# Optimization experiments

Measured on AMD Instinct MI355X. Metric: run time of the kernel, lower is better.

The kernel has to match this reference:

```python
import jax, jax.numpy as jnp
import numpy as np

EPS_F = 1e-6   # epsilon_F global in original repo
GAMMA = 0.8
K = 5
BN_EPS = 1e-5
M = 128
N = 100000
E = 1600000
MY = 10

def setup_inputs() -> dict:
    key = jax.random.key(0)
    ks = jax.random.split(key, 6)
    X = jax.random.normal(ks[0], (M, N), dtype=jnp.float32)
    # xavier_uniform for F: limit = sqrt(6/(m+m))
    lim = float(np.sqrt(6.0 / (M + M)))
    F_mat = jax.random.uniform(ks[1], (M, M), dtype=jnp.float32, minval=-lim, maxval=lim)
    B = (1.0 / np.sqrt(M)) * jax.random.normal(ks[2], (MY, M), dtype=jnp.float32)
    bn_weight = jnp.ones((M,), dtype=jnp.float32)
    bn_bias = jnp.zeros((M,), dtype=jnp.float32)
    edge_val = jax.random.uniform(ks[3], (E,), dtype=jnp.float32)
    edge_row = jax.random.randint(ks[4], (E,), 0, N, dtype=jnp.int64 if jax.config.jax_enable_x64 else jnp.int32)
    edge_col = jax.random.randint(ks[5], (E,), 0, N, dtype=jnp.int64 if jax.config.jax_enable_x64 else jnp.int32)
    return {"X": X, "F_mat": F_mat, "B": B, "bn_weight": bn_weight,
            "bn_bias": bn_bias, "edge_val": edge_val,
            "edge_row": edge_row, "edge_col": edge_col}

def reference(X, F_mat, B, bn_weight, bn_bias, edge_val, edge_row, edge_col):
    n = X.shape[1]
    # normalized Gram matrix g(F) = F^T F / (||F^T F||_fro + eps)
    FF = F_mat.T @ F_mat                       # [m, m]
    G = FF / (jnp.linalg.norm(FF) + EPS_F)
    X_first = X                                # [m, n]

    def step(Xc, _):
        Y = Xc.T                               # [n, m]
        # SpMM: (S_t @ Y)[r] += val * Y[c]
        SY = jax.ops.segment_sum(edge_val[:, None] * Y[edge_col], edge_row,
                                 num_segments=n)   # [n, m]
        Xn = GAMMA * (G @ SY.T) + X_first          # [m, n]
        return Xn, None

    Xk, _ = jax.lax.scan(step, X, None, length=K)
    out = Xk.T                                 # [n, m]
    # BatchNorm1d over feature dim (training-mode batch stats); dropout omitted (eval)
    mu = out.mean(axis=0)
    var = out.var(axis=0)
    out = (out - mu) * jax.lax.rsqrt(var + BN_EPS) * bn_weight + bn_bias
    return out @ B.T                           # [n, m_y]
```

## Files before the change

### kernel.cpp

```cpp
#include <hip/hip_runtime.h>
#include <math.h>

#define MDIM 128
#define MY 10
#define GAMMA 0.8f
#define KITER 5

__device__ __forceinline__ float bf2f(unsigned short h) {
    return __uint_as_float(((unsigned int)h) << 16);
}
__device__ __forceinline__ unsigned short f2bf(float f) {
    unsigned int u = __float_as_uint(f);
    u += 0x7fffu + ((u >> 16) & 1u);
    return (unsigned short)(u >> 16);
}

__global__ void k_transpose(const float* __restrict__ X, float* __restrict__ Y0,
                            unsigned short* __restrict__ Y0h, int n) {
    __shared__ float tile[32][33];
    int r0 = blockIdx.x * 32;
    int f0 = blockIdx.y * 32;
    int tx = threadIdx.x, ty = threadIdx.y;
    #pragma unroll
    for (int i = 0; i < 32; i += 8) {
        tile[ty + i][tx] = X[(size_t)(f0 + ty + i) * n + (r0 + tx)];
    }
    __syncthreads();
    #pragma unroll
    for (int i = 0; i < 32; i += 8) {
        float v = tile[tx][ty + i];
        Y0[(size_t)(r0 + ty + i) * MDIM + (f0 + tx)] = v;
        Y0h[(size_t)(r0 + ty + i) * MDIM + (f0 + tx)] = f2bf(v);
    }
}

__global__ void k_gram(const float* __restrict__ F, float* __restrict__ FF,
                       float* __restrict__ normAcc) {
    int i = blockIdx.x, j = threadIdx.x;
    float acc = 0.f;
    for (int k = 0; k < MDIM; ++k)
        acc = fmaf(F[k * MDIM + i], F[k * MDIM + j], acc);
    FF[i * MDIM + j] = acc;
    __shared__ float red[MDIM];
    red[j] = acc * acc;
    __syncthreads();
    for (int s = 64; s > 0; s >>= 1) {
        if (j < s) red[j] += red[j + s];
        __syncthreads();
    }
    if (j == 0) atomicAdd(normAcc, red[0]);
}

__global__ void k_gnorm(const float* __restrict__ FF, const float* __restrict__ normAcc,
                        float* __restrict__ G) {
    int idx = blockIdx.x * 256 + threadIdx.x;
    float s = GAMMA / (sqrtf(*normAcc) + 1e-6f);
    G[idx] = FF[idx] * s;
}

__global__ void k_hist(const int* __restrict__ erow, int* __restrict__ cnt, int E) {
    int e = blockIdx.x * 256 + threadIdx.x;
    if (e < E) atomicAdd(&cnt[erow[e]], 1);
}

__global__ void k_scan1(const int* __restrict__ cnt, int* __restrict__ blockSums, int n) {
    int tid = threadIdx.x;
    int base = blockIdx.x * 1024 + tid * 4;
    int s = 0;
    if (base + 3 < n) {
        int4 v = *(const int4*)&cnt[base];
        s = v.x + v.y + v.z + v.w;
    } else {
        for (int i = 0; i < 4; ++i)
            if (base + i < n) s += cnt[base + i];
    }
    __shared__ int red[256];
    red[tid] = s;
    __syncthreads();
    for (int st = 128; st > 0; st >>= 1) {
        if (tid < st) red[tid] += red[tid + st];
        __syncthreads();
    }
    if (tid == 0) blockSums[blockIdx.x] = red[0];
}

__global__ void k_scan2(int* __restrict__ blockSums, int* __restrict__ row_off,
                        int nb, int n) {
    __shared__ int s[256];
    int tid = threadIdx.x;
    int v = (tid < nb) ? blockSums[tid] : 0;
    s[tid] = v;
    __syncthreads();
    for (int off = 1; off < 256; off <<= 1) {
        int t = (tid >= off) ? s[tid - off] : 0;
        __syncthreads();
        s[tid] += t;
        __syncthreads();
    }
    if (tid < nb) blockSums[tid] = s[tid] - v;
    if (tid == 0) row_off[n] = s[255];
}

__global__ void k_scan3(const int* __restrict__ cnt, const int* __restrict__ blockOff,
                        int* __restrict__ row_off, int n) {
    int tid = threadIdx.x;
    int base = blockIdx.x * 1024 + tid * 4;
    int v[4];
    #pragma unroll
    for (int i = 0; i < 4; ++i) v[i] = (base + i < n) ? cnt[base + i] : 0;
    int local = v[0] + v[1] + v[2] + v[3];
    __shared__ int s[256];
    s[tid] = local;
    __syncthreads();
    for (int off = 1; off < 256; off <<= 1) {
        int t = (tid >= off) ? s[tid - off] : 0;
        __syncthreads();
        s[tid] += t;
        __syncthreads();
    }
    int excl = s[tid] - local + blockOff[blockIdx.x];
    #pragma unroll
    for (int i = 0; i < 4; ++i) {
        if (base + i < n) { row_off[base + i] = excl; excl += v[i]; }
    }
}

__global__ void k_scatter(const int* __restrict__ erow, const int* __restrict__ ecol,
                          const float* __restrict__ eval_, int* __restrict__ cursor,
                          int2* __restrict__ csr_cv, int E) {
    int e = blockIdx.x * 256 + threadIdx.x;
    if (e < E) {
        int r = erow[e];
        int pos = atomicAdd(&cursor[r], 1);
        csr_cv[pos] = make_int2(ecol[e], __float_as_int(eval_[e]));
    }
}

__global__ void __launch_bounds__(256, 8) k_fused(const unsigned short* __restrict__ Yh,
                                                  const int* __restrict__ row_off,
                                                  const int2* __restrict__ csr_cv,
                                                  const float* __restrict__ G,
                                                  const float* __restrict__ Y0,
                                                  float* __restrict__ Yout,
                                                  unsigned short* __restrict__ Yhout,
                                                  float* __restrict__ stats,
                                                  int writeH, int writeF, int n) {
    __shared__ float sSY[32 * MDIM];
    int tid = threadIdx.x;
    int ty = tid >> 5;
    int tx = tid & 31;
    int rbase = blockIdx.x * 32;

    for (int i = 0; i < 4; ++i) {
        int rloc = ty * 4 + i;
        int e0 = row_off[rbase + rloc];
        int e1 = row_off[rbase + rloc + 1];
        float4 a = make_float4(0.f, 0.f, 0.f, 0.f);
        int e = e0;
        for (; e + 4 <= e1; e += 4) {
            int2 p0 = csr_cv[e + 0];
            int2 p1 = csr_cv[e + 1];
            int2 p2 = csr_cv[e + 2];
            int2 p3 = csr_cv[e + 3];
            ushort4 h0 = *(const ushort4*)&Yh[(size_t)p0.x * MDIM + tx * 4];
            ushort4 h1 = *(const ushort4*)&Yh[(size_t)p1.x * MDIM + tx * 4];
            ushort4 h2 = *(const ushort4*)&Yh[(size_t)p2.x * MDIM + tx * 4];
            ushort4 h3 = *(const ushort4*)&Yh[(size_t)p3.x * MDIM + tx * 4];
            float v0 = __int_as_float(p0.y);
            float v1 = __int_as_float(p1.y);
            float v2 = __int_as_float(p2.y);
            float v3 = __int_as_float(p3.y);
            a.x = fmaf(v0, bf2f(h0.x), a.x);
            a.y = fmaf(v0, bf2f(h0.y), a.y);
            a.z = fmaf(v0, bf2f(h0.z), a.z);
            a.w = fmaf(v0, bf2f(h0.w), a.w);
            a.x = fmaf(v1, bf2f(h1.x), a.x);
            a.y = fmaf(v1, bf2f(h1.y), a.y);
            a.z = fmaf(v1, bf2f(h1.z), a.z);
            a.w = fmaf(v1, bf2f(h1.w), a.w);
            a.x = fmaf(v2, bf2f(h2.x), a.x);
            a.y = fmaf(v2, bf2f(h2.y), a.y);
            a.z = fmaf(v2, bf2f(h2.z), a.z);
            a.w = fmaf(v2, bf2f(h2.w), a.w);
            a.x = fmaf(v3, bf2f(h3.x), a.x);
            a.y = fmaf(v3, bf2f(h3.y), a.y);
            a.z = fmaf(v3, bf2f(h3.z), a.z);
            a.w = fmaf(v3, bf2f(h3.w), a.w);
        }
        for (; e < e1; ++e) {
            int2 p = csr_cv[e];
            float v = __int_as_float(p.y);
            ushort4 h = *(const ushort4*)&Yh[(size_t)p.x * MDIM + tx * 4];
            a.x = fmaf(v, bf2f(h.x), a.x);
            a.y = fmaf(v, bf2f(h.y), a.y);
            a.z = fmaf(v, bf2f(h.z), a.z);
            a.w = fmaf(v, bf2f(h.w), a.w);
        }
        *(float4*)&sSY[rloc * MDIM + tx * 4] = a;
    }

    size_t r0 = (size_t)rbase + ty * 4;
    int f0 = tx * 4;
    float4 acc[4];
    #pragma unroll
    for (int i = 0; i < 4; ++i) acc[i] = make_float4(0.f, 0.f, 0.f, 0.f);

    for (int j = 0; j < MDIM; j += 4) {
        float4 g0 = *(const float4*)&G[(j + 0) * MDIM + f0];
        float4 g1 = *(const float4*)&G[(j + 1) * MDIM + f0];
        float4 g2 = *(const float4*)&G[(j + 2) * MDIM + f0];
        float4 g3 = *(const float4*)&G[(j + 3) * MDIM + f0];
        #pragma unroll
        for (int i = 0; i < 4; ++i) {
            float4 sr = *(const float4*)&sSY[(ty * 4 + i) * MDIM + j];
            acc[i].x = fmaf(sr.x, g0.x, acc[i].x);
            acc[i].y = fmaf(sr.x, g0.y, acc[i].y);
            acc[i].z = fmaf(sr.x, g0.z, acc[i].z);
            acc[i].w = fmaf(sr.x, g0.w, acc[i].w);
            acc[i].x = fmaf(sr.y, g1.x, acc[i].x);
            acc[i].y = fmaf(sr.y, g1.y, acc[i].y);
            acc[i].z = fmaf(sr.y, g1.z, acc[i].z);
            acc[i].w = fmaf(sr.y, g1.w, acc[i].w);
            acc[i].x = fmaf(sr.z, g2.x, acc[i].x);
            acc[i].y = fmaf(sr.z, g2.y, acc[i].y);
            acc[i].z = fmaf(sr.z, g2.z, acc[i].z);
            acc[i].w = fmaf(sr.z, g2.w, acc[i].w);
            acc[i].x = fmaf(sr.w, g3.x, acc[i].x);
            acc[i].y = fmaf(sr.w, g3.y, acc[i].y);
            acc[i].z = fmaf(sr.w, g3.z, acc[i].z);
            acc[i].w = fmaf(sr.w, g3.w, acc[i].w);
        }
    }

    float4 bs = make_float4(0.f, 0.f, 0.f, 0.f);
    float4 bq = make_float4(0.f, 0.f, 0.f, 0.f);
    #pragma unroll
    for (int i = 0; i < 4; ++i) {
        float4 y0 = *(const float4*)&Y0[(r0 + i) * MDIM + f0];
        float4 o;
        o.x = acc[i].x + y0.x;
        o.y = acc[i].y + y0.y;
        o.z = acc[i].z + y0.z;
        o.w = acc[i].w + y0.w;
        if (writeF) {
            *(float4*)&Yout[(r0 + i) * MDIM + f0] = o;
            bs.x += o.x; bs.y += o.y; bs.z += o.z; bs.w += o.w;
            bq.x = fmaf(o.x, o.x, bq.x);
            bq.y = fmaf(o.y, o.y, bq.y);
            bq.z = fmaf(o.z, o.z, bq.z);
            bq.w = fmaf(o.w, o.w, bq.w);
        }
        if (writeH) {
            ushort4 h;
            h.x = f2bf(o.x);
            h.y = f2bf(o.y);
            h.z = f2bf(o.z);
            h.w = f2bf(o.w);
            *(ushort4*)&Yhout[(r0 + i) * MDIM + f0] = h;
        }
    }

    if (writeF) {
        __syncthreads();
        *(float4*)&sSY[ty * MDIM + f0] = bs;
        *(float4*)&sSY[8 * MDIM + ty * MDIM + f0] = bq;
        __syncthreads();
        if (tid < MDIM) {
            float a = 0.f, b = 0.f;
            #pragma unroll
            for (int t = 0; t < 8; ++t) {
                a += sSY[t * MDIM + tid];
                b += sSY[8 * MDIM + t * MDIM + tid];
            }
            atomicAdd(&stats[tid], a);
            atomicAdd(&stats[MDIM + tid], b);
        }
    }
}

__global__ void k_finalize(const float* __restrict__ stats, const float* __restrict__ B,
                           const float* __restrict__ bnw, const float* __restrict__ bnb,
                           float* __restrict__ Bs, float* __restrict__ cvec, int n) {
    int f = threadIdx.x;
    float inv_n = 1.f / (float)n;
    float mu = stats[f] * inv_n;
    float var = stats[MDIM + f] * inv_n - mu * mu;
    float rs = rsqrtf(var + 1e-5f);
    float sw = rs * bnw[f];
    float cv = bnb[f] - mu * sw;
    __shared__ float red[MDIM];
    for (int o = 0; o < MY; ++o) {
        float b = B[o * MDIM + f];
        Bs[o * MDIM + f] = b * sw;
        red[f] = b * cv;
        __syncthreads();
        for (int s = 64; s > 0; s >>= 1) {
            if (f < s) red[f] += red[f + s];
            __syncthreads();
        }
        if (f == 0) cvec[o] = red[0];
        __syncthreads();
    }
}

__global__ void __launch_bounds__(256) k_project(const float* __restrict__ Y,
                                                 const float* __restrict__ Bs,
                                                 const float* __restrict__ cvec,
                                                 float* __restrict__ out, int n) {
    __shared__ float yt[16 * 129];
    __shared__ float sB[MY * 129];
    __shared__ float sc[MY];
    int tid = threadIdx.x;
    size_t rbase = (size_t)blockIdx.x * 16;
    for (int idx = tid; idx < 16 * MDIM; idx += 256) {
        int r = idx >> 7, f = idx & 127;
        yt[r * 129 + f] = Y[(rbase + r) * MDIM + f];
    }
    for (int idx = tid; idx < MY * MDIM; idx += 256) {
        int o = idx >> 7, f = idx & 127;
        sB[o * 129 + f] = Bs[idx];
    }
    if (tid < MY) sc[tid] = cvec[tid];
    __syncthreads();
    if (tid < 16 * MY) {
        int r = tid / MY, o = tid % MY;
        float acc = sc[o];
        for (int f = 0; f < MDIM; ++f)
            acc = fmaf(yt[r * 129 + f], sB[o * 129 + f], acc);
        out[(rbase + r) * MY + o] = acc;
    }
}

extern "C" void kernel_launch(void* const* d_in, const int* in_sizes, int n_in,
                              void* d_out, int out_size, void* d_ws, size_t ws_size,
                              hipStream_t stream) {
    const float* X    = (const float*)d_in[0];
    const float* F    = (const float*)d_in[1];
    const float* B    = (const float*)d_in[2];
    const float* bnw  = (const float*)d_in[3];
    const float* bnb  = (const float*)d_in[4];
    const float* ev   = (const float*)d_in[5];
    const int*   erow = (const int*)d_in[6];
    const int*   ecol = (const int*)d_in[7];
    float* out = (float*)d_out;
    const int n = in_sizes[0] / MDIM;
    const int E = in_sizes[5];

    char* w = (char*)d_ws;
    size_t off = 0;
    auto carve = [&](size_t bytes) -> void* {
        void* p = w + off;
        off += (bytes + 255) & ~(size_t)255;
        return p;
    };
    float*          Y0    = (float*)carve((size_t)n * MDIM * 4);
    float*          Ycur  = (float*)carve((size_t)n * MDIM * 4);
    unsigned short* Yh_a  = (unsigned short*)carve((size_t)n * MDIM * 2);
    unsigned short* Yh_b  = (unsigned short*)carve((size_t)n * MDIM * 2);
    float* FF        = (float*)carve(MDIM * MDIM * 4);
    float* G         = (float*)carve(MDIM * MDIM * 4);
    int2*  csr_cv    = (int2*)carve((size_t)E * 8);
    int*   row_off   = (int*)carve((size_t)(n + 1) * 4);
    int*   cursor    = (int*)carve((size_t)n * 4);
    int*   cnt       = (int*)carve((size_t)n * 4);
    int*   blockSums = (int*)carve(1024 * 4);
    float* normAcc   = (float*)carve(4);
    float* stats     = (float*)carve(2 * MDIM * 4);
    float* Bs        = (float*)carve(MY * MDIM * 4);
    float* cvec      = (float*)carve(MY * 4);
    (void)ws_size;

    hipMemsetAsync(cnt, 0, (size_t)n * 4, stream);
    hipMemsetAsync(normAcc, 0, 4, stream);
    hipMemsetAsync(stats, 0, 2 * MDIM * 4, stream);

    k_transpose<<<dim3(n / 32, MDIM / 32), dim3(32, 8), 0, stream>>>(X, Y0, Yh_a, n);
    k_gram<<<MDIM, MDIM, 0, stream>>>(F, FF, normAcc);
    k_gnorm<<<MDIM * MDIM / 256, 256, 0, stream>>>(FF, normAcc, G);

    const int nb = (n + 1023) / 1024;
    k_hist<<<(E + 255) / 256, 256, 0, stream>>>(erow, cnt, E);
    k_scan1<<<nb, 256, 0, stream>>>(cnt, blockSums, n);
    k_scan2<<<1, 256, 0, stream>>>(blockSums, row_off, nb, n);
    k_scan3<<<nb, 256, 0, stream>>>(cnt, blockSums, row_off, n);
    hipMemcpyAsync(cursor, row_off, (size_t)n * 4, hipMemcpyDeviceToDevice, stream);
    k_scatter<<<(E + 255) / 256, 256, 0, stream>>>(erow, ecol, ev, cursor, csr_cv, E);

    for (int k = 0; k < KITER; ++k) {
        const unsigned short* hin = (k & 1) ? Yh_b : Yh_a;
        unsigned short*       hout = (k & 1) ? Yh_a : Yh_b;
        int writeH = (k < KITER - 1) ? 1 : 0;
        int writeF = (k == KITER - 1) ? 1 : 0;
        k_fused<<<n / 32, 256, 0, stream>>>(hin, row_off, csr_cv, G, Y0, Ycur, hout,
                                            stats, writeH, writeF, n);
    }

    k_finalize<<<1, MDIM, 0, stream>>>(stats, B, bnw, bnb, Bs, cvec, n);
    k_project<<<n / 16, 256, 0, stream>>>(Ycur, Bs, cvec, out, n);
}
```

Measured before the change: 920.4 us.

## Bucket CSR edges within each row by column chunk and prescale column byte offsets

```diff
diff --git a/kernel.cpp b/kernel.cpp
--- a/kernel.cpp
+++ b/kernel.cpp
@@ -5,6 +5,9 @@
 #define MY 10
 #define GAMMA 0.8f
 #define KITER 5
+#define CSHIFT 13
+#define CCHUNK 13
+#define SCAN_BLK 8192
 
 __device__ __forceinline__ float bf2f(unsigned short h) {
     return __uint_as_float(((unsigned int)h) << 16);
@@ -58,21 +61,25 @@
     G[idx] = FF[idx] * s;
 }
 
-__global__ void k_hist(const int* __restrict__ erow, int* __restrict__ cnt, int E) {
+__global__ void k_hist(const int* __restrict__ erow, const int* __restrict__ ecol,
+                       int* __restrict__ cnt, int E) {
     int e = blockIdx.x * 256 + threadIdx.x;
-    if (e < E) atomicAdd(&cnt[erow[e]], 1);
-}
-
-__global__ void k_scan1(const int* __restrict__ cnt, int* __restrict__ blockSums, int n) {
+    if (e < E) atomicAdd(&cnt[erow[e] * CCHUNK + (ecol[e] >> CSHIFT)], 1);
+}
+
+__global__ void k_scan1(const int* __restrict__ cnt, int* __restrict__ blockSums, int nC) {
     int tid = threadIdx.x;
-    int base = blockIdx.x * 1024 + tid * 4;
+    int base = blockIdx.x * SCAN_BLK + tid * 32;
     int s = 0;
-    if (base + 3 < n) {
-        int4 v = *(const int4*)&cnt[base];
-        s = v.x + v.y + v.z + v.w;
+    if (base + 31 < nC) {
+        #pragma unroll
+        for (int i = 0; i < 8; ++i) {
+            int4 v = *(const int4*)&cnt[base + i * 4];
+            s += v.x + v.y + v.z + v.w;
+        }
     } else {
-        for (int i = 0; i < 4; ++i)
-            if (base + i < n) s += cnt[base + i];
+        for (int i = 0; i < 32; ++i)
+            if (base + i < nC) s += cnt[base + i];
     }
     __shared__ int red[256];
     red[tid] = s;
@@ -84,8 +91,8 @@
     if (tid == 0) blockSums[blockIdx.x] = red[0];
 }
 
-__global__ void k_scan2(int* __restrict__ blockSums, int* __restrict__ row_off,
-                        int nb, int n) {
+__global__ void k_scan2(int* __restrict__ blockSums, int* __restrict__ rc_off,
+                        int nb, int nC) {
     __shared__ int s[256];
     int tid = threadIdx.x;
     int v = (tid < nb) ? blockSums[tid] : 0;
@@ -98,17 +105,19 @@
         __syncthreads();
     }
     if (tid < nb) blockSums[tid] = s[tid] - v;
-    if (tid == 0) row_off[n] = s[255];
+    if (tid == 0) rc_off[nC] = s[255];
 }
 
 __global__ void k_scan3(const int* __restrict__ cnt, const int* __restrict__ blockOff,
-                        int* __restrict__ row_off, int n) {
+                        int* __restrict__ rc_off, int nC) {
     int tid = threadIdx.x;
-    int base = blockIdx.x * 1024 + tid * 4;
-    int v[4];
-    #pragma unroll
-    for (int i = 0; i < 4; ++i) v[i] = (base + i < n) ? cnt[base + i] : 0;
-    int local = v[0] + v[1] + v[2] + v[3];
+    int base = blockIdx.x * SCAN_BLK + tid * 32;
+    int v[32];
+    #pragma unroll
+    for (int i = 0; i < 32; ++i) v[i] = (base + i < nC) ? cnt[base + i] : 0;
+    int local = 0;
+    #pragma unroll
+    for (int i = 0; i < 32; ++i) local += v[i];
     __shared__ int s[256];
     s[tid] = local;
     __syncthreads();
@@ -120,8 +129,8 @@
     }
     int excl = s[tid] - local + blockOff[blockIdx.x];
     #pragma unroll
-    for (int i = 0; i < 4; ++i) {
-        if (base + i < n) { row_off[base + i] = excl; excl += v[i]; }
+    for (int i = 0; i < 32; ++i) {
+        if (base + i < nC) { rc_off[base + i] = excl; excl += v[i]; }
     }
 }
 
@@ -131,13 +140,14 @@
     int e = blockIdx.x * 256 + threadIdx.x;
     if (e < E) {
         int r = erow[e];
-        int pos = atomicAdd(&cursor[r], 1);
-        csr_cv[pos] = make_int2(ecol[e], __float_as_int(eval_[e]));
+        int c = ecol[e];
+        int pos = atomicAdd(&cursor[r * CCHUNK + (c >> CSHIFT)], 1);
+        csr_cv[pos] = make_int2(c << 8, __float_as_int(eval_[e]));
     }
 }
 
 __global__ void __launch_bounds__(256, 8) k_fused(const unsigned short* __restrict__ Yh,
-                                                  const int* __restrict__ row_off,
+                                                  const int* __restrict__ rc_off,
                                                   const int2* __restrict__ csr_cv,
                                                   const float* __restrict__ G,
                                                   const float* __restrict__ Y0,
@@ -150,11 +160,13 @@
     int ty = tid >> 5;
     int tx = tid & 31;
     int rbase = blockIdx.x * 32;
+    const char* yb = (const char*)Yh;
+    int lbo = tx * 8;
 
     for (int i = 0; i < 4; ++i) {
         int rloc = ty * 4 + i;
-        int e0 = row_off[rbase + rloc];
-        int e1 = row_off[rbase + rloc + 1];
+        int e0 = rc_off[(rbase + rloc) * CCHUNK];
+        int e1 = rc_off[(rbase + rloc) * CCHUNK + CCHUNK];
         float4 a = make_float4(0.f, 0.f, 0.f, 0.f);
         int e = e0;
         for (; e + 4 <= e1; e += 4) {
@@ -162,10 +174,10 @@
             int2 p1 = csr_cv[e + 1];
             int2 p2 = csr_cv[e + 2];
             int2 p3 = csr_cv[e + 3];
-            ushort4 h0 = *(const ushort4*)&Yh[(size_t)p0.x * MDIM + tx * 4];
-            ushort4 h1 = *(const ushort4*)&Yh[(size_t)p1.x * MDIM + tx * 4];
-            ushort4 h2 = *(const ushort4*)&Yh[(size_t)p2.x * MDIM + tx * 4];
-            ushort4 h3 = *(const ushort4*)&Yh[(size_t)p3.x * MDIM + tx * 4];
+            ushort4 h0 = *(const ushort4*)(yb + (size_t)(p0.x + lbo));
+            ushort4 h1 = *(const ushort4*)(yb + (size_t)(p1.x + lbo));
+            ushort4 h2 = *(const ushort4*)(yb + (size_t)(p2.x + lbo));
+            ushort4 h3 = *(const ushort4*)(yb + (size_t)(p3.x + lbo));
             float v0 = __int_as_float(p0.y);
             float v1 = __int_as_float(p1.y);
             float v2 = __int_as_float(p2.y);
@@ -190,7 +202,7 @@
         for (; e < e1; ++e) {
             int2 p = csr_cv[e];
             float v = __int_as_float(p.y);
-            ushort4 h = *(const ushort4*)&Yh[(size_t)p.x * MDIM + tx * 4];
+            ushort4 h = *(const ushort4*)(yb + (size_t)(p.x + lbo));
             a.x = fmaf(v, bf2f(h.x), a.x);
             a.y = fmaf(v, bf2f(h.y), a.y);
             a.z = fmaf(v, bf2f(h.z), a.z);
@@ -345,6 +357,7 @@
     float* out = (float*)d_out;
     const int n = in_sizes[0] / MDIM;
     const int E = in_sizes[5];
+    const int nC = n * CCHUNK;
 
     char* w = (char*)d_ws;
     size_t off = 0;
@@ -360,9 +373,9 @@
     float* FF        = (float*)carve(MDIM * MDIM * 4);
     float* G         = (float*)carve(MDIM * MDIM * 4);
     int2*  csr_cv    = (int2*)carve((size_t)E * 8);
-    int*   row_off   = (int*)carve((size_t)(n + 1) * 4);
-    int*   cursor    = (int*)carve((size_t)n * 4);
-    int*   cnt       = (int*)carve((size_t)n * 4);
+    int*   rc_off    = (int*)carve((size_t)(nC + 1) * 4);
+    int*   cursor    = (int*)carve((size_t)nC * 4);
+    int*   cnt       = (int*)carve((size_t)nC * 4);
     int*   blockSums = (int*)carve(1024 * 4);
     float* normAcc   = (float*)carve(4);
     float* stats     = (float*)carve(2 * MDIM * 4);
@@ -370,7 +383,7 @@
     float* cvec      = (float*)carve(MY * 4);
     (void)ws_size;
 
-    hipMemsetAsync(cnt, 0, (size_t)n * 4, stream);
+    hipMemsetAsync(cnt, 0, (size_t)nC * 4, stream);
     hipMemsetAsync(normAcc, 0, 4, stream);
     hipMemsetAsync(stats, 0, 2 * MDIM * 4, stream);
 
@@ -378,12 +391,12 @@
     k_gram<<<MDIM, MDIM, 0, stream>>>(F, FF, normAcc);
     k_gnorm<<<MDIM * MDIM / 256, 256, 0, stream>>>(FF, normAcc, G);
 
-    const int nb = (n + 1023) / 1024;
-    k_hist<<<(E + 255) / 256, 256, 0, stream>>>(erow, cnt, E);
-    k_scan1<<<nb, 256, 0, stream>>>(cnt, blockSums, n);
-    k_scan2<<<1, 256, 0, stream>>>(blockSums, row_off, nb, n);
-    k_scan3<<<nb, 256, 0, stream>>>(cnt, blockSums, row_off, n);
-    hipMemcpyAsync(cursor, row_off, (size_t)n * 4, hipMemcpyDeviceToDevice, stream);
+    const int nb = (nC + SCAN_BLK - 1) / SCAN_BLK;
+    k_hist<<<(E + 255) / 256, 256, 0, stream>>>(erow, ecol, cnt, E);
+    k_scan1<<<nb, 256, 0, stream>>>(cnt, blockSums, nC);
+    k_scan2<<<1, 256, 0, stream>>>(blockSums, rc_off, nb, nC);
+    k_scan3<<<nb, 256, 0, stream>>>(cnt, blockSums, rc_off, nC);
+    hipMemcpyAsync(cursor, rc_off, (size_t)nC * 4, hipMemcpyDeviceToDevice, stream);
     k_scatter<<<(E + 255) / 256, 256, 0, stream>>>(erow, ecol, ev, cursor, csr_cv, E);
 
     for (int k = 0; k < KITER; ++k) {
@@ -391,7 +404,7 @@
         unsigned short*       hout = (k & 1) ? Yh_a : Yh_b;
         int writeH = (k < KITER - 1) ? 1 : 0;
         int writeF = (k == KITER - 1) ? 1 : 0;
-        k_fused<<<n / 32, 256, 0, stream>>>(hin, row_off, csr_cv, G, Y0, Ycur, hout,
+        k_fused<<<n / 32, 256, 0, stream>>>(hin, rc_off, csr_cv, G, Y0, Ycur, hout,
                                             stats, writeH, writeF, n);
     }
 
```

After: 934.0 us. About the same (+1.5%).

## Bucket CSR edges by row groups of four and gather with full-wavefront bf16x2 loads

Applied to the files above, without the earlier changes.

```diff
diff --git a/kernel.cpp b/kernel.cpp
--- a/kernel.cpp
+++ b/kernel.cpp
@@ -16,7 +16,8 @@
 }
 
 __global__ void k_transpose(const float* __restrict__ X, float* __restrict__ Y0,
-                            unsigned short* __restrict__ Y0h, int n) {
+                            unsigned short* __restrict__ Y0h,
+                            unsigned short* __restrict__ Yh0, int n) {
     __shared__ float tile[32][33];
     int r0 = blockIdx.x * 32;
     int f0 = blockIdx.y * 32;
@@ -29,8 +30,10 @@
     #pragma unroll
     for (int i = 0; i < 32; i += 8) {
         float v = tile[tx][ty + i];
+        unsigned short h = f2bf(v);
         Y0[(size_t)(r0 + ty + i) * MDIM + (f0 + tx)] = v;
-        Y0h[(size_t)(r0 + ty + i) * MDIM + (f0 + tx)] = f2bf(v);
+        Y0h[(size_t)(r0 + ty + i) * MDIM + (f0 + tx)] = h;
+        Yh0[(size_t)(r0 + ty + i) * MDIM + (f0 + tx)] = h;
     }
 }
 
@@ -125,80 +128,101 @@
     }
 }
 
+__global__ void k_cinit(const int* __restrict__ row_off, int* __restrict__ cursorB, int nbk) {
+    int b = blockIdx.x * 256 + threadIdx.x;
+    if (b < nbk) cursorB[b] = row_off[b << 2];
+}
+
 __global__ void k_scatter(const int* __restrict__ erow, const int* __restrict__ ecol,
-                          const float* __restrict__ eval_, int* __restrict__ cursor,
+                          const float* __restrict__ eval_, int* __restrict__ cursorB,
                           int2* __restrict__ csr_cv, int E) {
     int e = blockIdx.x * 256 + threadIdx.x;
     if (e < E) {
         int r = erow[e];
-        int pos = atomicAdd(&cursor[r], 1);
-        csr_cv[pos] = make_int2(ecol[e], __float_as_int(eval_[e]));
-    }
-}
+        int c = ecol[e];
+        int pos = atomicAdd(&cursorB[r >> 2], 1);
+        csr_cv[pos] = make_int2((c << 8) | (r & 3), __float_as_int(eval_[e]));
+    }
+}
+
+#define EDGE(p, h, A0, A1, A2, A3)                                          \
+    {                                                                       \
+        float v = __int_as_float(p.y);                                      \
+        float f0 = __uint_as_float(((unsigned)h) << 16);                    \
+        float f1 = __uint_as_float(((unsigned)h) & 0xFFFF0000u);            \
+        int rid = __builtin_amdgcn_readfirstlane(p.x) & 3;                  \
+        if (rid == 0)      { A0.x = fmaf(v, f0, A0.x); A0.y = fmaf(v, f1, A0.y); } \
+        else if (rid == 1) { A1.x = fmaf(v, f0, A1.x); A1.y = fmaf(v, f1, A1.y); } \
+        else if (rid == 2) { A2.x = fmaf(v, f0, A2.x); A2.y = fmaf(v, f1, A2.y); } \
+        else               { A3.x = fmaf(v, f0, A3.x); A3.y = fmaf(v, f1, A3.y); } \
+    }
+
+#define GATHER_BUCKET(BK, A0, A1, A2, A3)                                   \
+    {                                                                       \
+        int e  = row_off[(BK) << 2];                                        \
+        int e1 = row_off[((BK) << 2) + 4];                                  \
+        for (; e + 8 <= e1; e += 8) {                                       \
+            int2 p0 = csr_cv[e + 0]; int2 p1 = csr_cv[e + 1];               \
+            int2 p2 = csr_cv[e + 2]; int2 p3 = csr_cv[e + 3];               \
+            int2 p4 = csr_cv[e + 4]; int2 p5 = csr_cv[e + 5];               \
+            int2 p6 = csr_cv[e + 6]; int2 p7 = csr_cv[e + 7];               \
+            unsigned h0 = *(const unsigned*)(yb + (size_t)((p0.x & 0xFFFFFF00) + lbo)); \
+            unsigned h1 = *(const unsigned*)(yb + (size_t)((p1.x & 0xFFFFFF00) + lbo)); \
+            unsigned h2 = *(const unsigned*)(yb + (size_t)((p2.x & 0xFFFFFF00) + lbo)); \
+            unsigned h3 = *(const unsigned*)(yb + (size_t)((p3.x & 0xFFFFFF00) + lbo)); \
+            unsigned h4 = *(const unsigned*)(yb + (size_t)((p4.x & 0xFFFFFF00) + lbo)); \
+            unsigned h5 = *(const unsigned*)(yb + (size_t)((p5.x & 0xFFFFFF00) + lbo)); \
+            unsigned h6 = *(const unsigned*)(yb + (size_t)((p6.x & 0xFFFFFF00) + lbo)); \
+            unsigned h7 = *(const unsigned*)(yb + (size_t)((p7.x & 0xFFFFFF00) + lbo)); \
+            EDGE(p0, h0, A0, A1, A2, A3) EDGE(p1, h1, A0, A1, A2, A3)       \
+            EDGE(p2, h2, A0, A1, A2, A3) EDGE(p3, h3, A0, A1, A2, A3)       \
+            EDGE(p4, h4, A0, A1, A2, A3) EDGE(p5, h5, A0, A1, A2, A3)       \
+            EDGE(p6, h6, A0, A1, A2, A3) EDGE(p7, h7, A0, A1, A2, A3)       \
+        }                                                                   \
+        for (; e < e1; ++e) {                                               \
+            int2 p = csr_cv[e];                                             \
+            unsigned h = *(const unsigned*)(yb + (size_t)((p.x & 0xFFFFFF00) + lbo)); \
+            EDGE(p, h, A0, A1, A2, A3)                                      \
+        }                                                                   \
+    }
 
 __global__ void __launch_bounds__(256, 8) k_fused(const unsigned short* __restrict__ Yh,
                                                   const int* __restrict__ row_off,
                                                   const int2* __restrict__ csr_cv,
                                                   const float* __restrict__ G,
                                                   const float* __restrict__ Y0,
+                                                  const unsigned short* __restrict__ Y0h,
                                                   float* __restrict__ Yout,
                                                   unsigned short* __restrict__ Yhout,
                                                   float* __restrict__ stats,
                                                   int writeH, int writeF, int n) {
     __shared__ float sSY[32 * MDIM];
     int tid = threadIdx.x;
+    int lane = tid & 63;
+    int w = tid >> 6;
+    int rbase = blockIdx.x * 32;
+    const char* yb = (const char*)Yh;
+    int lbo = lane * 4;
+
+    float2 z = make_float2(0.f, 0.f);
+    float2 a0 = z, a1 = z, a2 = z, a3 = z;
+    float2 b0 = z, b1 = z, b2 = z, b3 = z;
+
+    int bk0 = (rbase >> 2) + 2 * w;
+    GATHER_BUCKET(bk0,     a0, a1, a2, a3)
+    GATHER_BUCKET(bk0 + 1, b0, b1, b2, b3)
+
+    *(float2*)&sSY[(w * 8 + 0) * MDIM + lane * 2] = a0;
+    *(float2*)&sSY[(w * 8 + 1) * MDIM + lane * 2] = a1;
+    *(float2*)&sSY[(w * 8 + 2) * MDIM + lane * 2] = a2;
+    *(float2*)&sSY[(w * 8 + 3) * MDIM + lane * 2] = a3;
+    *(float2*)&sSY[(w * 8 + 4) * MDIM + lane * 2] = b0;
+    *(float2*)&sSY[(w * 8 + 5) * MDIM + lane * 2] = b1;
+    *(float2*)&sSY[(w * 8 + 6) * MDIM + lane * 2] = b2;
+    *(float2*)&sSY[(w * 8 + 7) * MDIM + lane * 2] = b3;
+
     int ty = tid >> 5;
     int tx = tid & 31;
-    int rbase = blockIdx.x * 32;
-
-    for (int i = 0; i < 4; ++i) {
-        int rloc = ty * 4 + i;
-        int e0 = row_off[rbase + rloc];
-        int e1 = row_off[rbase + rloc + 1];
-        float4 a = make_float4(0.f, 0.f, 0.f, 0.f);
-        int e = e0;
-        for (; e + 4 <= e1; e += 4) {
-            int2 p0 = csr_cv[e + 0];
-            int2 p1 = csr_cv[e + 1];
-            int2 p2 = csr_cv[e + 2];
-            int2 p3 = csr_cv[e + 3];
-            ushort4 h0 = *(const ushort4*)&Yh[(size_t)p0.x * MDIM + tx * 4];
-            ushort4 h1 = *(const ushort4*)&Yh[(size_t)p1.x * MDIM + tx * 4];
-            ushort4 h2 = *(const ushort4*)&Yh[(size_t)p2.x * MDIM + tx * 4];
-            ushort4 h3 = *(const ushort4*)&Yh[(size_t)p3.x * MDIM + tx * 4];
-            float v0 = __int_as_float(p0.y);
-            float v1 = __int_as_float(p1.y);
-            float v2 = __int_as_float(p2.y);
-            float v3 = __int_as_float(p3.y);
-            a.x = fmaf(v0, bf2f(h0.x), a.x);
-            a.y = fmaf(v0, bf2f(h0.y), a.y);
-            a.z = fmaf(v0, bf2f(h0.z), a.z);
-            a.w = fmaf(v0, bf2f(h0.w), a.w);
-            a.x = fmaf(v1, bf2f(h1.x), a.x);
-            a.y = fmaf(v1, bf2f(h1.y), a.y);
-            a.z = fmaf(v1, bf2f(h1.z), a.z);
-            a.w = fmaf(v1, bf2f(h1.w), a.w);
-            a.x = fmaf(v2, bf2f(h2.x), a.x);
-            a.y = fmaf(v2, bf2f(h2.y), a.y);
-            a.z = fmaf(v2, bf2f(h2.z), a.z);
-            a.w = fmaf(v2, bf2f(h2.w), a.w);
-            a.x = fmaf(v3, bf2f(h3.x), a.x);
-            a.y = fmaf(v3, bf2f(h3.y), a.y);
-            a.z = fmaf(v3, bf2f(h3.z), a.z);
-            a.w = fmaf(v3, bf2f(h3.w), a.w);
-        }
-        for (; e < e1; ++e) {
-            int2 p = csr_cv[e];
-            float v = __int_as_float(p.y);
-            ushort4 h = *(const ushort4*)&Yh[(size_t)p.x * MDIM + tx * 4];
-            a.x = fmaf(v, bf2f(h.x), a.x);
-            a.y = fmaf(v, bf2f(h.y), a.y);
-            a.z = fmaf(v, bf2f(h.z), a.z);
-            a.w = fmaf(v, bf2f(h.w), a.w);
-        }
-        *(float4*)&sSY[rloc * MDIM + tx * 4] = a;
-    }
-
     size_t r0 = (size_t)rbase + ty * 4;
     int f0 = tx * 4;
     float4 acc[4];
@@ -236,7 +260,16 @@
     float4 bq = make_float4(0.f, 0.f, 0.f, 0.f);
     #pragma unroll
     for (int i = 0; i < 4; ++i) {
-        float4 y0 = *(const float4*)&Y0[(r0 + i) * MDIM + f0];
+        float4 y0;
+        if (writeF) {
+            y0 = *(const float4*)&Y0[(r0 + i) * MDIM + f0];
+        } else {
+            ushort4 t4 = *(const ushort4*)&Y0h[(r0 + i) * MDIM + f0];
+            y0.x = bf2f(t4.x);
+            y0.y = bf2f(t4.y);
+            y0.z = bf2f(t4.z);
+            y0.w = bf2f(t4.w);
+        }
         float4 o;
         o.x = acc[i].x + y0.x;
         o.y = acc[i].y + y0.y;
@@ -345,6 +378,7 @@
     float* out = (float*)d_out;
     const int n = in_sizes[0] / MDIM;
     const int E = in_sizes[5];
+    const int nbk = (n + 3) / 4;
 
     char* w = (char*)d_ws;
     size_t off = 0;
@@ -355,13 +389,14 @@
     };
     float*          Y0    = (float*)carve((size_t)n * MDIM * 4);
     float*          Ycur  = (float*)carve((size_t)n * MDIM * 4);
+    unsigned short* Y0h   = (unsigned short*)carve((size_t)n * MDIM * 2);
     unsigned short* Yh_a  = (unsigned short*)carve((size_t)n * MDIM * 2);
     unsigned short* Yh_b  = (unsigned short*)carve((size_t)n * MDIM * 2);
     float* FF        = (float*)carve(MDIM * MDIM * 4);
     float* G         = (float*)carve(MDIM * MDIM * 4);
     int2*  csr_cv    = (int2*)carve((size_t)E * 8);
     int*   row_off   = (int*)carve((size_t)(n + 1) * 4);
-    int*   cursor    = (int*)carve((size_t)n * 4);
+    int*   cursorB   = (int*)carve((size_t)nbk * 4);
     int*   cnt       = (int*)carve((size_t)n * 4);
     int*   blockSums = (int*)carve(1024 * 4);
     float* normAcc   = (float*)carve(4);
@@ -374,7 +409,7 @@
     hipMemsetAsync(normAcc, 0, 4, stream);
     hipMemsetAsync(stats, 0, 2 * MDIM * 4, stream);
 
-    k_transpose<<<dim3(n / 32, MDIM / 32), dim3(32, 8), 0, stream>>>(X, Y0, Yh_a, n);
+    k_transpose<<<dim3(n / 32, MDIM / 32), dim3(32, 8), 0, stream>>>(X, Y0, Y0h, Yh_a, n);
     k_gram<<<MDIM, MDIM, 0, stream>>>(F, FF, normAcc);
     k_gnorm<<<MDIM * MDIM / 256, 256, 0, stream>>>(FF, normAcc, G);
 
@@ -383,16 +418,16 @@
     k_scan1<<<nb, 256, 0, stream>>>(cnt, blockSums, n);
     k_scan2<<<1, 256, 0, stream>>>(blockSums, row_off, nb, n);
     k_scan3<<<nb, 256, 0, stream>>>(cnt, blockSums, row_off, n);
-    hipMemcpyAsync(cursor, row_off, (size_t)n * 4, hipMemcpyDeviceToDevice, stream);
-    k_scatter<<<(E + 255) / 256, 256, 0, stream>>>(erow, ecol, ev, cursor, csr_cv, E);
+    k_cinit<<<(nbk + 255) / 256, 256, 0, stream>>>(row_off, cursorB, nbk);
+    k_scatter<<<(E + 255) / 256, 256, 0, stream>>>(erow, ecol, ev, cursorB, csr_cv, E);
 
     for (int k = 0; k < KITER; ++k) {
         const unsigned short* hin = (k & 1) ? Yh_b : Yh_a;
         unsigned short*       hout = (k & 1) ? Yh_a : Yh_b;
         int writeH = (k < KITER - 1) ? 1 : 0;
         int writeF = (k == KITER - 1) ? 1 : 0;
-        k_fused<<<n / 32, 256, 0, stream>>>(hin, row_off, csr_cv, G, Y0, Ycur, hout,
-                                            stats, writeH, writeF, n);
+        k_fused<<<(n + 31) / 32, 256, 0, stream>>>(hin, row_off, csr_cv, G, Y0, Y0h,
+                                                   Ycur, hout, stats, writeH, writeF, n);
     }
 
     k_finalize<<<1, MDIM, 0, stream>>>(stats, B, bnw, bnb, Bs, cvec, n);
```

Result: slower. 1.154 ms (+25.4%).

## Gather bf16 rows with 16-byte loads and drop fp32 intermediate buffers

Applied to the files above, without the earlier changes.

```diff
diff --git a/kernel.cpp b/kernel.cpp
--- a/kernel.cpp
+++ b/kernel.cpp
@@ -16,7 +16,8 @@
 }
 
 __global__ void k_transpose(const float* __restrict__ X, float* __restrict__ Y0,
-                            unsigned short* __restrict__ Y0h, int n) {
+                            unsigned short* __restrict__ Y0h,
+                            unsigned short* __restrict__ Yh0, int n) {
     __shared__ float tile[32][33];
     int r0 = blockIdx.x * 32;
     int f0 = blockIdx.y * 32;
@@ -29,8 +30,10 @@
     #pragma unroll
     for (int i = 0; i < 32; i += 8) {
         float v = tile[tx][ty + i];
+        unsigned short h = f2bf(v);
         Y0[(size_t)(r0 + ty + i) * MDIM + (f0 + tx)] = v;
-        Y0h[(size_t)(r0 + ty + i) * MDIM + (f0 + tx)] = f2bf(v);
+        Y0h[(size_t)(r0 + ty + i) * MDIM + (f0 + tx)] = h;
+        Yh0[(size_t)(r0 + ty + i) * MDIM + (f0 + tx)] = h;
     }
 }
 
@@ -102,7 +105,7 @@
 }
 
 __global__ void k_scan3(const int* __restrict__ cnt, const int* __restrict__ blockOff,
-                        int* __restrict__ row_off, int n) {
+                        int* __restrict__ row_off, int* __restrict__ cursor, int n) {
     int tid = threadIdx.x;
     int base = blockIdx.x * 1024 + tid * 4;
     int v[4];
@@ -121,7 +124,11 @@
     int excl = s[tid] - local + blockOff[blockIdx.x];
     #pragma unroll
     for (int i = 0; i < 4; ++i) {
-        if (base + i < n) { row_off[base + i] = excl; excl += v[i]; }
+        if (base + i < n) {
+            row_off[base + i] = excl;
+            cursor[base + i] = excl;
+            excl += v[i];
+        }
     }
 }
 
@@ -131,74 +138,79 @@
     int e = blockIdx.x * 256 + threadIdx.x;
     if (e < E) {
         int r = erow[e];
+        int c = ecol[e];
         int pos = atomicAdd(&cursor[r], 1);
-        csr_cv[pos] = make_int2(ecol[e], __float_as_int(eval_[e]));
-    }
-}
+        csr_cv[pos] = make_int2(c << 8, __float_as_int(eval_[e]));
+    }
+}
+
+#define FMA8(v, q)                                                         \
+    A.x  = fmaf(v, __uint_as_float(((unsigned)(q).x) << 16), A.x);         \
+    A.y  = fmaf(v, __uint_as_float(((unsigned)(q).x) & 0xFFFF0000u), A.y); \
+    A.z  = fmaf(v, __uint_as_float(((unsigned)(q).y) << 16), A.z);         \
+    A.w  = fmaf(v, __uint_as_float(((unsigned)(q).y) & 0xFFFF0000u), A.w); \
+    Bv.x = fmaf(v, __uint_as_float(((unsigned)(q).z) << 16), Bv.x);        \
+    Bv.y = fmaf(v, __uint_as_float(((unsigned)(q).z) & 0xFFFF0000u), Bv.y);\
+    Bv.z = fmaf(v, __uint_as_float(((unsigned)(q).w) << 16), Bv.z);        \
+    Bv.w = fmaf(v, __uint_as_float(((unsigned)(q).w) & 0xFFFF0000u), Bv.w);
 
 __global__ void __launch_bounds__(256, 8) k_fused(const unsigned short* __restrict__ Yh,
                                                   const int* __restrict__ row_off,
                                                   const int2* __restrict__ csr_cv,
                                                   const float* __restrict__ G,
                                                   const float* __restrict__ Y0,
-                                                  float* __restrict__ Yout,
+                                                  const unsigned short* __restrict__ Y0h,
                                                   unsigned short* __restrict__ Yhout,
                                                   float* __restrict__ stats,
-                                                  int writeH, int writeF, int n) {
+                                                  int writeF, int n) {
     __shared__ float sSY[32 * MDIM];
     int tid = threadIdx.x;
+    int rbase = blockIdx.x * 32;
+    const char* yb = (const char*)Yh;
+
+    {
+        int g16 = tid >> 4;
+        int l16 = tid & 15;
+        int lbo = l16 * 16;
+        #pragma unroll
+        for (int j = 0; j < 2; ++j) {
+            int rloc = g16 * 2 + j;
+            int e0 = row_off[rbase + rloc];
+            int e1 = row_off[rbase + rloc + 1];
+            float4 A  = make_float4(0.f, 0.f, 0.f, 0.f);
+            float4 Bv = make_float4(0.f, 0.f, 0.f, 0.f);
+            int e = e0;
+            for (; e + 4 <= e1; e += 4) {
+                int2 p0 = csr_cv[e + 0];
+                int2 p1 = csr_cv[e + 1];
+                int2 p2 = csr_cv[e + 2];
+                int2 p3 = csr_cv[e + 3];
+                int4 q0 = *(const int4*)(yb + (size_t)(p0.x + lbo));
+                int4 q1 = *(const int4*)(yb + (size_t)(p1.x + lbo));
+                int4 q2 = *(const int4*)(yb + (size_t)(p2.x + lbo));
+                int4 q3 = *(const int4*)(yb + (size_t)(p3.x + lbo));
+                float v0 = __int_as_float(p0.y);
+                float v1 = __int_as_float(p1.y);
+                float v2 = __int_as_float(p2.y);
+                float v3 = __int_as_float(p3.y);
+                FMA8(v0, q0)
+                FMA8(v1, q1)
+                FMA8(v2, q2)
+                FMA8(v3, q3)
+            }
+            for (; e < e1; ++e) {
+                int2 p = csr_cv[e];
+                int4 q = *(const int4*)(yb + (size_t)(p.x + lbo));
+                float v = __int_as_float(p.y);
+                FMA8(v, q)
+            }
+            *(float4*)&sSY[rloc * MDIM + l16 * 8] = A;
+            *(float4*)&sSY[rloc * MDIM + l16 * 8 + 4] = Bv;
+        }
+    }
+
     int ty = tid >> 5;
     int tx = tid & 31;
-    int rbase = blockIdx.x * 32;
-
-    for (int i = 0; i < 4; ++i) {
-        int rloc = ty * 4 + i;
-        int e0 = row_off[rbase + rloc];
-        int e1 = row_off[rbase + rloc + 1];
-        float4 a = make_float4(0.f, 0.f, 0.f, 0.f);
-        int e = e0;
-        for (; e + 4 <= e1; e += 4) {
-            int2 p0 = csr_cv[e + 0];
-            int2 p1 = csr_cv[e + 1];
-            int2 p2 = csr_cv[e + 2];
-            int2 p3 = csr_cv[e + 3];
-            ushort4 h0 = *(const ushort4*)&Yh[(size_t)p0.x * MDIM + tx * 4];
-            ushort4 h1 = *(const ushort4*)&Yh[(size_t)p1.x * MDIM + tx * 4];
-            ushort4 h2 = *(const ushort4*)&Yh[(size_t)p2.x * MDIM + tx * 4];
-            ushort4 h3 = *(const ushort4*)&Yh[(size_t)p3.x * MDIM + tx * 4];
-            float v0 = __int_as_float(p0.y);
-            float v1 = __int_as_float(p1.y);
-            float v2 = __int_as_float(p2.y);
-            float v3 = __int_as_float(p3.y);
-            a.x = fmaf(v0, bf2f(h0.x), a.x);
-            a.y = fmaf(v0, bf2f(h0.y), a.y);
-            a.z = fmaf(v0, bf2f(h0.z), a.z);
-            a.w = fmaf(v0, bf2f(h0.w), a.w);
-            a.x = fmaf(v1, bf2f(h1.x), a.x);
-            a.y = fmaf(v1, bf2f(h1.y), a.y);
-            a.z = fmaf(v1, bf2f(h1.z), a.z);
-            a.w = fmaf(v1, bf2f(h1.w), a.w);
-            a.x = fmaf(v2, bf2f(h2.x), a.x);
-            a.y = fmaf(v2, bf2f(h2.y), a.y);
-            a.z = fmaf(v2, bf2f(h2.z), a.z);
-            a.w = fmaf(v2, bf2f(h2.w), a.w);
-            a.x = fmaf(v3, bf2f(h3.x), a.x);
-            a.y = fmaf(v3, bf2f(h3.y), a.y);
-            a.z = fmaf(v3, bf2f(h3.z), a.z);
-            a.w = fmaf(v3, bf2f(h3.w), a.w);
-        }
-        for (; e < e1; ++e) {
-            int2 p = csr_cv[e];
-            float v = __int_as_float(p.y);
-            ushort4 h = *(const ushort4*)&Yh[(size_t)p.x * MDIM + tx * 4];
-            a.x = fmaf(v, bf2f(h.x), a.x);
-            a.y = fmaf(v, bf2f(h.y), a.y);
-            a.z = fmaf(v, bf2f(h.z), a.z);
-            a.w = fmaf(v, bf2f(h.w), a.w);
-        }
-        *(float4*)&sSY[rloc * MDIM + tx * 4] = a;
-    }
-
     size_t r0 = (size_t)rbase + ty * 4;
     int f0 = tx * 4;
     float4 acc[4];
@@ -236,28 +248,34 @@
     float4 bq = make_float4(0.f, 0.f, 0.f, 0.f);
     #pragma unroll
     for (int i = 0; i < 4; ++i) {
-        float4 y0 = *(const float4*)&Y0[(r0 + i) * MDIM + f0];
+        float4 y0;
+        if (writeF) {
+            y0 = *(const float4*)&Y0[(r0 + i) * MDIM + f0];
+        } else {
+            ushort4 t4 = *(const ushort4*)&Y0h[(r0 + i) * MDIM + f0];
+            y0.x = bf2f(t4.x);
+            y0.y = bf2f(t4.y);
+            y0.z = bf2f(t4.z);
+            y0.w = bf2f(t4.w);
+        }
         float4 o;
         o.x = acc[i].x + y0.x;
         o.y = acc[i].y + y0.y;
         o.z = acc[i].z + y0.z;
         o.w = acc[i].w + y0.w;
         if (writeF) {
-            *(float4*)&Yout[(r0 + i) * MDIM + f0] = o;
             bs.x += o.x; bs.y += o.y; bs.z += o.z; bs.w += o.w;
             bq.x = fmaf(o.x, o.x, bq.x);
             bq.y = fmaf(o.y, o.y, bq.y);
             bq.z = fmaf(o.z, o.z, bq.z);
             bq.w = fmaf(o.w, o.w, bq.w);
         }
-        if (writeH) {
-            ushort4 h;
-            h.x = f2bf(o.x);
-            h.y = f2bf(o.y);
-            h.z = f2bf(o.z);
-            h.w = f2bf(o.w);
-            *(ushort4*)&Yhout[(r0 + i) * MDIM + f0] = h;
-        }
+        ushort4 h;
+        h.x = f2bf(o.x);
+        h.y = f2bf(o.y);
+        h.z = f2bf(o.z);
+        h.w = f2bf(o.w);
+        *(ushort4*)&Yhout[(r0 + i) * MDIM + f0] = h;
     }
 
     if (writeF) {
@@ -303,7 +321,7 @@
     }
 }
 
-__global__ void __launch_bounds__(256) k_project(const float* __restrict__ Y,
+__global__ void __launch_bounds__(256) k_project(const unsigned short* __restrict__ Yh,
                                                  const float* __restrict__ Bs,
                                                  const float* __restrict__ cvec,
                                                  float* __restrict__ out, int n) {
@@ -312,9 +330,14 @@
     __shared__ float sc[MY];
     int tid = threadIdx.x;
     size_t rbase = (size_t)blockIdx.x * 16;
-    for (int idx = tid; idx < 16 * MDIM; idx += 256) {
-        int r = idx >> 7, f = idx & 127;
-        yt[r * 129 + f] = Y[(rbase + r) * MDIM + f];
+    for (int idx = tid; idx < 16 * MDIM / 4; idx += 256) {
+        int r = idx >> 5;
+        int f = (idx & 31) * 4;
+        ushort4 h = *(const ushort4*)&Yh[(rbase + r) * MDIM + f];
+        yt[r * 129 + f + 0] = bf2f(h.x);
+        yt[r * 129 + f + 1] = bf2f(h.y);
+        yt[r * 129 + f + 2] = bf2f(h.z);
+        yt[r * 129 + f + 3] = bf2f(h.w);
     }
     for (int idx = tid; idx < MY * MDIM; idx += 256) {
         int o = idx >> 7, f = idx & 127;
@@ -354,7 +377,7 @@
         return p;
     };
     float*          Y0    = (float*)carve((size_t)n * MDIM * 4);
-    float*          Ycur  = (float*)carve((size_t)n * MDIM * 4);
+    unsigned short* Y0h   = (unsigned short*)carve((size_t)n * MDIM * 2);
     unsigned short* Yh_a  = (unsigned short*)carve((size_t)n * MDIM * 2);
     unsigned short* Yh_b  = (unsigned short*)carve((size_t)n * MDIM * 2);
     float* FF        = (float*)carve(MDIM * MDIM * 4);
@@ -374,7 +397,7 @@
     hipMemsetAsync(normAcc, 0, 4, stream);
     hipMemsetAsync(stats, 0, 2 * MDIM * 4, stream);
 
-    k_transpose<<<dim3(n / 32, MDIM / 32), dim3(32, 8), 0, stream>>>(X, Y0, Yh_a, n);
+    k_transpose<<<dim3(n / 32, MDIM / 32), dim3(32, 8), 0, stream>>>(X, Y0, Y0h, Yh_a, n);
     k_gram<<<MDIM, MDIM, 0, stream>>>(F, FF, normAcc);
     k_gnorm<<<MDIM * MDIM / 256, 256, 0, stream>>>(FF, normAcc, G);
 
@@ -382,19 +405,18 @@
     k_hist<<<(E + 255) / 256, 256, 0, stream>>>(erow, cnt, E);
     k_scan1<<<nb, 256, 0, stream>>>(cnt, blockSums, n);
     k_scan2<<<1, 256, 0, stream>>>(blockSums, row_off, nb, n);
-    k_scan3<<<nb, 256, 0, stream>>>(cnt, blockSums, row_off, n);
-    hipMemcpyAsync(cursor, row_off, (size_t)n * 4, hipMemcpyDeviceToDevice, stream);
+    k_scan3<<<nb, 256, 0, stream>>>(cnt, blockSums, row_off, cursor, n);
     k_scatter<<<(E + 255) / 256, 256, 0, stream>>>(erow, ecol, ev, cursor, csr_cv, E);
 
     for (int k = 0; k < KITER; ++k) {
         const unsigned short* hin = (k & 1) ? Yh_b : Yh_a;
         unsigned short*       hout = (k & 1) ? Yh_a : Yh_b;
-        int writeH = (k < KITER - 1) ? 1 : 0;
         int writeF = (k == KITER - 1) ? 1 : 0;
-        k_fused<<<n / 32, 256, 0, stream>>>(hin, row_off, csr_cv, G, Y0, Ycur, hout,
-                                            stats, writeH, writeF, n);
-    }
-
+        k_fused<<<(n + 31) / 32, 256, 0, stream>>>(hin, row_off, csr_cv, G, Y0, Y0h,
+                                                   hout, stats, writeF, n);
+    }
+
+    const unsigned short* Yfinal = (KITER & 1) ? Yh_b : Yh_a;
     k_finalize<<<1, MDIM, 0, stream>>>(stats, B, bnw, bnb, Bs, cvec, n);
-    k_project<<<n / 16, 256, 0, stream>>>(Ycur, Bs, cvec, out, n);
-}
+    k_project<<<n / 16, 256, 0, stream>>>(Yfinal, Bs, cvec, out, n);
+}
```

Result: slower. 1.094 ms (+18.9%).
